# Optimization experiments

Measured on AMD Instinct MI355X. Metric: run time of the kernel, lower is better.

Reference implementation:

```python
import jax, jax.numpy as jnp
import numpy as np
from jax import lax

B, L = 2, 8192
HIDDEN = 2048
HEADS = 16
DPH = HIDDEN // HEADS          # hidden_size_per_attention_head = 128
STATE = 8                      # state_size
GROUPS = HIDDEN                # hyena_filter_groups == num_systems (per-channel filters)
K = 3                          # short_filter_length


def setup_inputs() -> dict:
    key = jax.random.key(0)
    ks = jax.random.split(key, 6)
    u = jax.random.normal(ks[0], (B, L, 3 * HIDDEN), jnp.float32)
    short_filter_weight = jax.random.normal(ks[1], (3 * HIDDEN, 1, K), jnp.float32) * 0.2
    short_filter_bias = jax.random.normal(ks[2], (3 * HIDDEN,), jnp.float32) * 0.1
    # poles must be stable (negative log-pole) so exp(log_pole * t) stays finite for t up to L
    log_poles = -jax.random.uniform(ks[3], (GROUPS, STATE, 1), jnp.float32, 1e-3, 0.1)
    residues = jax.random.normal(ks[4], (GROUPS, STATE), jnp.float32) * (1.0 / STATE)
    D = jax.random.normal(ks[5], (HIDDEN,), jnp.float32) * 0.1
    return {"u": u, "short_filter_weight": short_filter_weight,
            "short_filter_bias": short_filter_bias, "log_poles": log_poles,
            "residues": residues, "D": D}


def _column_split(z):
    # z: [B, 3*HIDDEN, L] -> head-wise split into x2, x1, v each [B, HIDDEN, L]
    b, _, l = z.shape
    z = z.reshape(b, HEADS, 3 * DPH, l)
    x2 = z[:, :, :DPH].reshape(b, HIDDEN, l)
    x1 = z[:, :, DPH:2 * DPH].reshape(b, HIDDEN, l)
    v = z[:, :, 2 * DPH:].reshape(b, HIDDEN, l)
    return x2, x1, v


def _forward(u, short_filter_weight, short_filter_bias, log_poles, residues, D):
    # ---- parallel_fir: causal depthwise short conv over 3*HIDDEN channels ----
    uc = jnp.transpose(u, (0, 2, 1))  # [B, 3D, L]
    z_pre = lax.conv_general_dilated(
        uc, short_filter_weight, window_strides=(1,), padding=[(K - 1, 0)],
        dimension_numbers=("NCH", "OIH", "NCH"), feature_group_count=3 * HIDDEN)
    z_pre = z_pre + short_filter_bias[None, :, None]  # [B, 3D, L]

    # ---- compute_filter: pole/residue SSM -> implicit long filter h [1, G, L] ----
    t = jnp.arange(L, dtype=jnp.float32)[None, None]            # [1, 1, L]
    kern = jnp.exp(log_poles * t)                               # [G, S, L]
    h = jnp.einsum("gs,gsl->gl", residues, kern)[None]          # [1, G, L]
    # repeat_interleave(hidden//groups = 1, dim=0) is a no-op when GROUPS == HIDDEN

    # ---- parallel_iir: column split, gating, FFT circular conv ----
    x2, x1, v = _column_split(z_pre)
    x1v = x1 * v                                                # [B, D, L]

    fft_size = 2 * L
    H = jnp.fft.rfft(h.astype(jnp.float32), n=fft_size) / fft_size
    X = jnp.fft.rfft(x1v.astype(jnp.float32), n=fft_size)
    y = jnp.fft.irfft(X * H, n=fft_size, norm="forward")[..., :L]
    y = (y.astype(x1v.dtype) + x1v * D[:, None]) * x2           # [B, D, L]
    return jnp.transpose(y, (0, 2, 1))                          # [B, L, D]


def reference(u, short_filter_weight, short_filter_bias, log_poles, residues, D):
    return _forward(u, short_filter_weight, short_filter_bias, log_poles, residues, D)
```

## Files before the change

### kernel.cpp

```cpp
#include <hip/hip_runtime.h>
#include <cstddef>

namespace {
constexpr int kB   = 2;
constexpr int kL   = 8192;
constexpr int kHid = 2048;
constexpr int kC3  = 6144;
constexpr int kS   = 8;
constexpr int kNC  = 64;
constexpr int kCL  = kL / kNC;
}

__global__ __launch_bounds__(256) void hyena_pass1(
    const float* __restrict__ u, const float* __restrict__ w,
    const float* __restrict__ bias, const float* __restrict__ lp,
    float* __restrict__ A)
{
  const int d  = blockIdx.x * 256 + threadIdx.x;
  const int ch = blockIdx.y;
  const int b  = blockIdx.z;
  const int head = d >> 7, r = d & 127;
  const int c1 = head * 384 + 128 + r;
  const int cv = head * 384 + 256 + r;

  const float w10 = w[c1*3+0], w11 = w[c1*3+1], w12 = w[c1*3+2], b1 = bias[c1];
  const float wv0 = w[cv*3+0], wv1 = w[cv*3+1], wv2 = w[cv*3+2], bv = bias[cv];

  float p[kS];
  #pragma unroll
  for (int j = 0; j < kS; ++j) p[j] = expf(lp[d*kS + j]);

  const int l0 = ch * kCL;
  const float* ub = u + (size_t)b * kL * kC3;

  float u1m2 = 0.f, u1m1 = 0.f, uvm2 = 0.f, uvm1 = 0.f;
  if (l0 >= 2) { u1m2 = ub[(size_t)(l0-2)*kC3 + c1]; uvm2 = ub[(size_t)(l0-2)*kC3 + cv]; }
  if (l0 >= 1) { u1m1 = ub[(size_t)(l0-1)*kC3 + c1]; uvm1 = ub[(size_t)(l0-1)*kC3 + cv]; }

  float s[kS];
  #pragma unroll
  for (int j = 0; j < kS; ++j) s[j] = 0.f;

  #pragma unroll 4
  for (int l = l0; l < l0 + kCL; ++l) {
    const float u1 = ub[(size_t)l*kC3 + c1];
    const float uv = ub[(size_t)l*kC3 + cv];
    const float x1 = fmaf(w10, u1m2, fmaf(w11, u1m1, fmaf(w12, u1, b1)));
    const float v  = fmaf(wv0, uvm2, fmaf(wv1, uvm1, fmaf(wv2, uv, bv)));
    const float x  = x1 * v;
    #pragma unroll
    for (int j = 0; j < kS; ++j) s[j] = fmaf(p[j], s[j], x);
    u1m2 = u1m1; u1m1 = u1; uvm2 = uvm1; uvm1 = uv;
  }

  float* Ad = A + (((size_t)b*kNC + ch)*kHid + d) * kS;
  #pragma unroll
  for (int j = 0; j < kS; ++j) Ad[j] = s[j];
}

__global__ __launch_bounds__(256) void hyena_pass2(
    const float* __restrict__ lp, float* __restrict__ A)
{
  const int t = blockIdx.x * 256 + threadIdx.x;
  const int j = t & (kS - 1);
  const int d = (t >> 3) & (kHid - 1);
  const int b = t >> 14;
  const float pC = expf(lp[d*kS + j] * (float)kCL);

  const size_t base   = (size_t)b * kNC * kHid * kS + (size_t)d * kS + j;
  const size_t stride = (size_t)kHid * kS;

  float s = 0.f;
  for (int c0 = 0; c0 < kNC; c0 += 8) {
    float a[8];
    #pragma unroll
    for (int k = 0; k < 8; ++k) a[k] = A[base + (size_t)(c0 + k) * stride];
    #pragma unroll
    for (int k = 0; k < 8; ++k) {
      s = fmaf(pC, s, a[k]);
      A[base + (size_t)(c0 + k) * stride] = s;
    }
  }
}

__global__ __launch_bounds__(256) void hyena_pass3(
    const float* __restrict__ u, const float* __restrict__ w,
    const float* __restrict__ bias, const float* __restrict__ lp,
    const float* __restrict__ res, const float* __restrict__ Dv,
    const float* __restrict__ A, float* __restrict__ out)
{
  const int d  = blockIdx.x * 256 + threadIdx.x;
  const int ch = blockIdx.y;
  const int b  = blockIdx.z;
  const int head = d >> 7, r = d & 127;
  const int c2 = head * 384 + r;
  const int c1 = c2 + 128;
  const int cv = c2 + 256;

  const float w20 = w[c2*3+0], w21 = w[c2*3+1], w22 = w[c2*3+2], b2 = bias[c2];
  const float w10 = w[c1*3+0], w11 = w[c1*3+1], w12 = w[c1*3+2], b1 = bias[c1];
  const float wv0 = w[cv*3+0], wv1 = w[cv*3+1], wv2 = w[cv*3+2], bv = bias[cv];
  const float Dd = Dv[d];

  float p[kS], rr[kS], s[kS];
  #pragma unroll
  for (int j = 0; j < kS; ++j) {
    p[j]  = expf(lp[d*kS + j]);
    rr[j] = res[d*kS + j];
  }
  if (ch == 0) {
    #pragma unroll
    for (int j = 0; j < kS; ++j) s[j] = 0.f;
  } else {
    const float* Ad = A + (((size_t)b*kNC + (ch - 1))*kHid + d) * kS;
    #pragma unroll
    for (int j = 0; j < kS; ++j) s[j] = Ad[j];
  }

  const int l0 = ch * kCL;
  const float* ub = u + (size_t)b * kL * kC3;

  float u2m2 = 0.f, u2m1 = 0.f, u1m2 = 0.f, u1m1 = 0.f, uvm2 = 0.f, uvm1 = 0.f;
  if (l0 >= 2) {
    u2m2 = ub[(size_t)(l0-2)*kC3 + c2];
    u1m2 = ub[(size_t)(l0-2)*kC3 + c1];
    uvm2 = ub[(size_t)(l0-2)*kC3 + cv];
  }
  if (l0 >= 1) {
    u2m1 = ub[(size_t)(l0-1)*kC3 + c2];
    u1m1 = ub[(size_t)(l0-1)*kC3 + c1];
    uvm1 = ub[(size_t)(l0-1)*kC3 + cv];
  }

  float* ob = out + (size_t)b * kL * kHid + d;

  #pragma unroll 4
  for (int l = l0; l < l0 + kCL; ++l) {
    const float u2 = ub[(size_t)l*kC3 + c2];
    const float u1 = ub[(size_t)l*kC3 + c1];
    const float uv = ub[(size_t)l*kC3 + cv];
    const float x2 = fmaf(w20, u2m2, fmaf(w21, u2m1, fmaf(w22, u2, b2)));
    const float x1 = fmaf(w10, u1m2, fmaf(w11, u1m1, fmaf(w12, u1, b1)));
    const float v  = fmaf(wv0, uvm2, fmaf(wv1, uvm1, fmaf(wv2, uv, bv)));
    const float x  = x1 * v;
    #pragma unroll
    for (int j = 0; j < kS; ++j) s[j] = fmaf(p[j], s[j], x);
    float y = 0.f;
    #pragma unroll
    for (int j = 0; j < kS; ++j) y = fmaf(rr[j], s[j], y);
    ob[(size_t)l * kHid] = fmaf(x, Dd, y) * x2;
    u2m2 = u2m1; u2m1 = u2; u1m2 = u1m1; u1m1 = u1; uvm2 = uvm1; uvm1 = uv;
  }
}

extern "C" void kernel_launch(void* const* d_in, const int* in_sizes, int n_in,
                              void* d_out, int out_size, void* d_ws, size_t ws_size,
                              hipStream_t stream) {
  const float* u    = (const float*)d_in[0];
  const float* w    = (const float*)d_in[1];
  const float* bias = (const float*)d_in[2];
  const float* lp   = (const float*)d_in[3];
  const float* res  = (const float*)d_in[4];
  const float* Dv   = (const float*)d_in[5];
  float* out = (float*)d_out;
  float* A   = (float*)d_ws;

  const dim3 blk(256);
  const dim3 g13(kHid / 256, kNC, kB);
  hipLaunchKernelGGL(hyena_pass1, g13, blk, 0, stream, u, w, bias, lp, A);
  hipLaunchKernelGGL(hyena_pass2, dim3((kB * kHid * kS) / 256), blk, 0, stream, lp, A);
  hipLaunchKernelGGL(hyena_pass3, g13, blk, 0, stream, u, w, bias, lp, res, Dv, A, out);
}
```

Baseline: 632.1 us.

## Process two channels per thread with float2 loads and double-buffered row prefetch

New measurement: 631.4 us. About the same (-0.1%).

```diff
diff --git a/kernel.cpp b/kernel.cpp
--- a/kernel.cpp
+++ b/kernel.cpp
@@ -1,5 +1,6 @@
 #include <hip/hip_runtime.h>
 #include <cstddef>
+#include <cstdint>
 
 namespace {
 constexpr int kB   = 2;
@@ -9,6 +10,8 @@
 constexpr int kS   = 8;
 constexpr int kNC  = 64;
 constexpr int kCL  = kL / kNC;
+constexpr int kRB  = 4;
+constexpr int kNB  = kCL / kRB;
 }
 
 __global__ __launch_bounds__(256) void hyena_pass1(
@@ -16,46 +19,100 @@
     const float* __restrict__ bias, const float* __restrict__ lp,
     float* __restrict__ A)
 {
-  const int d  = blockIdx.x * 256 + threadIdx.x;
-  const int ch = blockIdx.y;
-  const int b  = blockIdx.z;
-  const int head = d >> 7, r = d & 127;
-  const int c1 = head * 384 + 128 + r;
-  const int cv = head * 384 + 256 + r;
-
-  const float w10 = w[c1*3+0], w11 = w[c1*3+1], w12 = w[c1*3+2], b1 = bias[c1];
-  const float wv0 = w[cv*3+0], wv1 = w[cv*3+1], wv2 = w[cv*3+2], bv = bias[cv];
-
-  float p[kS];
-  #pragma unroll
-  for (int j = 0; j < kS; ++j) p[j] = expf(lp[d*kS + j]);
+  const int tid  = threadIdx.x;
+  const int ch   = blockIdx.y;
+  const int b    = blockIdx.z;
+  const int head = blockIdx.x * 4 + (tid >> 6);
+  const int r2   = (tid & 63) * 2;
+  const int d0   = head * 128 + r2;
+  const int c1   = head * 384 + 128 + r2;
+  const int cv   = c1 + 128;
+
+  float w1k[2][3], wvk[2][3], b1[2], bv[2];
+  #pragma unroll
+  for (int q = 0; q < 2; ++q) {
+    #pragma unroll
+    for (int k = 0; k < 3; ++k) {
+      w1k[q][k] = w[(c1 + q) * 3 + k];
+      wvk[q][k] = w[(cv + q) * 3 + k];
+    }
+    b1[q] = bias[c1 + q];
+    bv[q] = bias[cv + q];
+  }
+
+  float p[2][kS], s[2][kS];
+  #pragma unroll
+  for (int q = 0; q < 2; ++q)
+    #pragma unroll
+    for (int j = 0; j < kS; ++j) {
+      p[q][j] = expf(lp[(d0 + q) * kS + j]);
+      s[q][j] = 0.f;
+    }
 
   const int l0 = ch * kCL;
   const float* ub = u + (size_t)b * kL * kC3;
 
-  float u1m2 = 0.f, u1m1 = 0.f, uvm2 = 0.f, uvm1 = 0.f;
-  if (l0 >= 2) { u1m2 = ub[(size_t)(l0-2)*kC3 + c1]; uvm2 = ub[(size_t)(l0-2)*kC3 + cv]; }
-  if (l0 >= 1) { u1m1 = ub[(size_t)(l0-1)*kC3 + c1]; uvm1 = ub[(size_t)(l0-1)*kC3 + cv]; }
-
-  float s[kS];
-  #pragma unroll
-  for (int j = 0; j < kS; ++j) s[j] = 0.f;
-
-  #pragma unroll 4
-  for (int l = l0; l < l0 + kCL; ++l) {
-    const float u1 = ub[(size_t)l*kC3 + c1];
-    const float uv = ub[(size_t)l*kC3 + cv];
-    const float x1 = fmaf(w10, u1m2, fmaf(w11, u1m1, fmaf(w12, u1, b1)));
-    const float v  = fmaf(wv0, uvm2, fmaf(wv1, uvm1, fmaf(wv2, uv, bv)));
-    const float x  = x1 * v;
-    #pragma unroll
-    for (int j = 0; j < kS; ++j) s[j] = fmaf(p[j], s[j], x);
-    u1m2 = u1m1; u1m1 = u1; uvm2 = uvm1; uvm1 = uv;
-  }
-
-  float* Ad = A + (((size_t)b*kNC + ch)*kHid + d) * kS;
-  #pragma unroll
-  for (int j = 0; j < kS; ++j) Ad[j] = s[j];
+  float m2_1[2] = {0.f, 0.f}, m1_1[2] = {0.f, 0.f};
+  float m2_v[2] = {0.f, 0.f}, m1_v[2] = {0.f, 0.f};
+  if (l0 >= 2) {
+    float2 t1 = *(const float2*)&ub[(size_t)(l0 - 2) * kC3 + c1];
+    float2 tv = *(const float2*)&ub[(size_t)(l0 - 2) * kC3 + cv];
+    m2_1[0] = t1.x; m2_1[1] = t1.y; m2_v[0] = tv.x; m2_v[1] = tv.y;
+  }
+  if (l0 >= 1) {
+    float2 t1 = *(const float2*)&ub[(size_t)(l0 - 1) * kC3 + c1];
+    float2 tv = *(const float2*)&ub[(size_t)(l0 - 1) * kC3 + cv];
+    m1_1[0] = t1.x; m1_1[1] = t1.y; m1_v[0] = tv.x; m1_v[1] = tv.y;
+  }
+
+  const float* up = ub + (size_t)l0 * kC3;
+
+  float2 a1A[kRB], avA[kRB], a1B[kRB], avB[kRB];
+
+  auto loadb = [&](float2 (&a1)[kRB], float2 (&av)[kRB], int t) {
+    const float* rp = up + (size_t)t * kRB * kC3;
+    #pragma unroll
+    for (int k = 0; k < kRB; ++k) {
+      a1[k] = *(const float2*)&rp[(size_t)k * kC3 + c1];
+      av[k] = *(const float2*)&rp[(size_t)k * kC3 + cv];
+    }
+  };
+
+  auto comp = [&](const float2 (&a1)[kRB], const float2 (&av)[kRB]) {
+    #pragma unroll
+    for (int k = 0; k < kRB; ++k) {
+      const float c1v[2] = {a1[k].x, a1[k].y};
+      const float cvv[2] = {av[k].x, av[k].y};
+      #pragma unroll
+      for (int q = 0; q < 2; ++q) {
+        const float x1 = fmaf(w1k[q][0], m2_1[q],
+                         fmaf(w1k[q][1], m1_1[q],
+                         fmaf(w1k[q][2], c1v[q], b1[q])));
+        const float v  = fmaf(wvk[q][0], m2_v[q],
+                         fmaf(wvk[q][1], m1_v[q],
+                         fmaf(wvk[q][2], cvv[q], bv[q])));
+        const float x = x1 * v;
+        #pragma unroll
+        for (int j = 0; j < kS; ++j) s[q][j] = fmaf(p[q][j], s[q][j], x);
+        m2_1[q] = m1_1[q]; m1_1[q] = c1v[q];
+        m2_v[q] = m1_v[q]; m1_v[q] = cvv[q];
+      }
+    }
+  };
+
+  loadb(a1A, avA, 0);
+  for (int t = 0; t < kNB; t += 2) {
+    if (t + 1 < kNB) loadb(a1B, avB, t + 1);
+    comp(a1A, avA);
+    if (t + 2 < kNB) loadb(a1A, avA, t + 2);
+    comp(a1B, avB);
+  }
+
+  float* Ad = A + (((size_t)b * kNC + ch) * kHid + d0) * kS;
+  #pragma unroll
+  for (int q = 0; q < 2; ++q)
+    #pragma unroll
+    for (int j = 0; j < kS; ++j) Ad[q * kS + j] = s[q][j];
 }
 
 __global__ __launch_bounds__(256) void hyena_pass2(
@@ -89,67 +146,132 @@
     const float* __restrict__ res, const float* __restrict__ Dv,
     const float* __restrict__ A, float* __restrict__ out)
 {
-  const int d  = blockIdx.x * 256 + threadIdx.x;
-  const int ch = blockIdx.y;
-  const int b  = blockIdx.z;
-  const int head = d >> 7, r = d & 127;
-  const int c2 = head * 384 + r;
-  const int c1 = c2 + 128;
-  const int cv = c2 + 256;
-
-  const float w20 = w[c2*3+0], w21 = w[c2*3+1], w22 = w[c2*3+2], b2 = bias[c2];
-  const float w10 = w[c1*3+0], w11 = w[c1*3+1], w12 = w[c1*3+2], b1 = bias[c1];
-  const float wv0 = w[cv*3+0], wv1 = w[cv*3+1], wv2 = w[cv*3+2], bv = bias[cv];
-  const float Dd = Dv[d];
-
-  float p[kS], rr[kS], s[kS];
-  #pragma unroll
-  for (int j = 0; j < kS; ++j) {
-    p[j]  = expf(lp[d*kS + j]);
-    rr[j] = res[d*kS + j];
-  }
+  const int tid  = threadIdx.x;
+  const int ch   = blockIdx.y;
+  const int b    = blockIdx.z;
+  const int head = blockIdx.x * 4 + (tid >> 6);
+  const int r2   = (tid & 63) * 2;
+  const int d0   = head * 128 + r2;
+  const int c2   = head * 384 + r2;
+  const int c1   = c2 + 128;
+  const int cv   = c2 + 256;
+
+  float w2k[2][3], w1k[2][3], wvk[2][3], b2[2], b1[2], bv[2], Dd[2];
+  #pragma unroll
+  for (int q = 0; q < 2; ++q) {
+    #pragma unroll
+    for (int k = 0; k < 3; ++k) {
+      w2k[q][k] = w[(c2 + q) * 3 + k];
+      w1k[q][k] = w[(c1 + q) * 3 + k];
+      wvk[q][k] = w[(cv + q) * 3 + k];
+    }
+    b2[q] = bias[c2 + q];
+    b1[q] = bias[c1 + q];
+    bv[q] = bias[cv + q];
+    Dd[q] = Dv[d0 + q];
+  }
+
+  float p[2][kS], rr[2][kS], s[2][kS];
+  #pragma unroll
+  for (int q = 0; q < 2; ++q)
+    #pragma unroll
+    for (int j = 0; j < kS; ++j) {
+      p[q][j]  = expf(lp[(d0 + q) * kS + j]);
+      rr[q][j] = res[(d0 + q) * kS + j];
+    }
   if (ch == 0) {
     #pragma unroll
-    for (int j = 0; j < kS; ++j) s[j] = 0.f;
+    for (int q = 0; q < 2; ++q)
+      #pragma unroll
+      for (int j = 0; j < kS; ++j) s[q][j] = 0.f;
   } else {
-    const float* Ad = A + (((size_t)b*kNC + (ch - 1))*kHid + d) * kS;
-    #pragma unroll
-    for (int j = 0; j < kS; ++j) s[j] = Ad[j];
+    const float* Ad = A + (((size_t)b * kNC + (ch - 1)) * kHid + d0) * kS;
+    #pragma unroll
+    for (int q = 0; q < 2; ++q)
+      #pragma unroll
+      for (int j = 0; j < kS; ++j) s[q][j] = Ad[q * kS + j];
   }
 
   const int l0 = ch * kCL;
   const float* ub = u + (size_t)b * kL * kC3;
 
-  float u2m2 = 0.f, u2m1 = 0.f, u1m2 = 0.f, u1m1 = 0.f, uvm2 = 0.f, uvm1 = 0.f;
+  float m2_2[2] = {0.f, 0.f}, m1_2[2] = {0.f, 0.f};
+  float m2_1[2] = {0.f, 0.f}, m1_1[2] = {0.f, 0.f};
+  float m2_v[2] = {0.f, 0.f}, m1_v[2] = {0.f, 0.f};
   if (l0 >= 2) {
-    u2m2 = ub[(size_t)(l0-2)*kC3 + c2];
-    u1m2 = ub[(size_t)(l0-2)*kC3 + c1];
-    uvm2 = ub[(size_t)(l0-2)*kC3 + cv];
+    float2 t2 = *(const float2*)&ub[(size_t)(l0 - 2) * kC3 + c2];
+    float2 t1 = *(const float2*)&ub[(size_t)(l0 - 2) * kC3 + c1];
+    float2 tv = *(const float2*)&ub[(size_t)(l0 - 2) * kC3 + cv];
+    m2_2[0] = t2.x; m2_2[1] = t2.y;
+    m2_1[0] = t1.x; m2_1[1] = t1.y;
+    m2_v[0] = tv.x; m2_v[1] = tv.y;
   }
   if (l0 >= 1) {
-    u2m1 = ub[(size_t)(l0-1)*kC3 + c2];
-    u1m1 = ub[(size_t)(l0-1)*kC3 + c1];
-    uvm1 = ub[(size_t)(l0-1)*kC3 + cv];
-  }
-
-  float* ob = out + (size_t)b * kL * kHid + d;
-
-  #pragma unroll 4
-  for (int l = l0; l < l0 + kCL; ++l) {
-    const float u2 = ub[(size_t)l*kC3 + c2];
-    const float u1 = ub[(size_t)l*kC3 + c1];
-    const float uv = ub[(size_t)l*kC3 + cv];
-    const float x2 = fmaf(w20, u2m2, fmaf(w21, u2m1, fmaf(w22, u2, b2)));
-    const float x1 = fmaf(w10, u1m2, fmaf(w11, u1m1, fmaf(w12, u1, b1)));
-    const float v  = fmaf(wv0, uvm2, fmaf(wv1, uvm1, fmaf(wv2, uv, bv)));
-    const float x  = x1 * v;
-    #pragma unroll
-    for (int j = 0; j < kS; ++j) s[j] = fmaf(p[j], s[j], x);
-    float y = 0.f;
-    #pragma unroll
-    for (int j = 0; j < kS; ++j) y = fmaf(rr[j], s[j], y);
-    ob[(size_t)l * kHid] = fmaf(x, Dd, y) * x2;
-    u2m2 = u2m1; u2m1 = u2; u1m2 = u1m1; u1m1 = u1; uvm2 = uvm1; uvm1 = uv;
+    float2 t2 = *(const float2*)&ub[(size_t)(l0 - 1) * kC3 + c2];
+    float2 t1 = *(const float2*)&ub[(size_t)(l0 - 1) * kC3 + c1];
+    float2 tv = *(const float2*)&ub[(size_t)(l0 - 1) * kC3 + cv];
+    m1_2[0] = t2.x; m1_2[1] = t2.y;
+    m1_1[0] = t1.x; m1_1[1] = t1.y;
+    m1_v[0] = tv.x; m1_v[1] = tv.y;
+  }
+
+  const float* up = ub + (size_t)l0 * kC3;
+  float* ob = out + ((size_t)b * kL + l0) * kHid + d0;
+
+  float2 a2A[kRB], a1A[kRB], avA[kRB];
+  float2 a2B[kRB], a1B[kRB], avB[kRB];
+
+  auto loadb = [&](float2 (&a2)[kRB], float2 (&a1)[kRB], float2 (&av)[kRB],
+                   int t) {
+    const float* rp = up + (size_t)t * kRB * kC3;
+    #pragma unroll
+    for (int k = 0; k < kRB; ++k) {
+      a2[k] = *(const float2*)&rp[(size_t)k * kC3 + c2];
+      a1[k] = *(const float2*)&rp[(size_t)k * kC3 + c1];
+      av[k] = *(const float2*)&rp[(size_t)k * kC3 + cv];
+    }
+  };
+
+  auto comp = [&](const float2 (&a2)[kRB], const float2 (&a1)[kRB],
+                  const float2 (&av)[kRB], int t) {
+    #pragma unroll
+    for (int k = 0; k < kRB; ++k) {
+      const float c2v[2] = {a2[k].x, a2[k].y};
+      const float c1v[2] = {a1[k].x, a1[k].y};
+      const float cvv[2] = {av[k].x, av[k].y};
+      float o[2];
+      #pragma unroll
+      for (int q = 0; q < 2; ++q) {
+        const float x2 = fmaf(w2k[q][0], m2_2[q],
+                         fmaf(w2k[q][1], m1_2[q],
+                         fmaf(w2k[q][2], c2v[q], b2[q])));
+        const float x1 = fmaf(w1k[q][0], m2_1[q],
+                         fmaf(w1k[q][1], m1_1[q],
+                         fmaf(w1k[q][2], c1v[q], b1[q])));
+        const float v  = fmaf(wvk[q][0], m2_v[q],
+                         fmaf(wvk[q][1], m1_v[q],
+                         fmaf(wvk[q][2], cvv[q], bv[q])));
+        const float x = x1 * v;
+        #pragma unroll
+        for (int j = 0; j < kS; ++j) s[q][j] = fmaf(p[q][j], s[q][j], x);
+        float y = 0.f;
+        #pragma unroll
+        for (int j = 0; j < kS; ++j) y = fmaf(rr[q][j], s[q][j], y);
+        o[q] = fmaf(x, Dd[q], y) * x2;
+        m2_2[q] = m1_2[q]; m1_2[q] = c2v[q];
+        m2_1[q] = m1_1[q]; m1_1[q] = c1v[q];
+        m2_v[q] = m1_v[q]; m1_v[q] = cvv[q];
+      }
+      *(float2*)&ob[(size_t)(t * kRB + k) * kHid] = make_float2(o[0], o[1]);
+    }
+  };
+
+  loadb(a2A, a1A, avA, 0);
+  for (int t = 0; t < kNB; t += 2) {
+    if (t + 1 < kNB) loadb(a2B, a1B, avB, t + 1);
+    comp(a2A, a1A, avA, t);
+    if (t + 2 < kNB) loadb(a2A, a1A, avA, t + 2);
+    comp(a2B, a1B, avB, t + 1);
   }
 }
 
@@ -166,7 +288,7 @@
   float* A   = (float*)d_ws;
 
   const dim3 blk(256);
-  const dim3 g13(kHid / 256, kNC, kB);
+  const dim3 g13(kHid / 512, kNC, kB);
   hipLaunchKernelGGL(hyena_pass1, g13, blk, 0, stream, u, w, bias, lp, A);
   hipLaunchKernelGGL(hyena_pass2, dim3((kB * kHid * kS) / 256), blk, 0, stream, lp, A);
   hipLaunchKernelGGL(hyena_pass3, g13, blk, 0, stream, u, w, bias, lp, res, Dv, A, out);
```

## Fuse three scan passes into one kernel with grid barrier and fp16-cached gated input

Applied to the files above, without the earlier changes.

New measurement: 785.7 us. 24.3% more time.

```diff
diff --git a/kernel.cpp b/kernel.cpp
--- a/kernel.cpp
+++ b/kernel.cpp
@@ -1,155 +1,145 @@
 #include <hip/hip_runtime.h>
+#include <hip/hip_fp16.h>
 #include <cstddef>
+#include <cstdint>
 
 namespace {
-constexpr int kB   = 2;
-constexpr int kL   = 8192;
-constexpr int kHid = 2048;
-constexpr int kC3  = 6144;
-constexpr int kS   = 8;
-constexpr int kNC  = 64;
-constexpr int kCL  = kL / kNC;
+constexpr int kB    = 2;
+constexpr int kL    = 8192;
+constexpr int kHid  = 2048;
+constexpr int kC3   = 6144;
+constexpr int kS    = 8;
+constexpr int kNC   = 32;
+constexpr int kCL   = kL / kNC;
+constexpr int kPair = kCL / 2;
+constexpr unsigned kNBlk = kB * kNC * 8;
 }
 
-__global__ __launch_bounds__(256) void hyena_pass1(
+__global__ __launch_bounds__(256, 2) void hyena_fused(
     const float* __restrict__ u, const float* __restrict__ w,
     const float* __restrict__ bias, const float* __restrict__ lp,
-    float* __restrict__ A)
+    const float* __restrict__ res, const float* __restrict__ Dv,
+    float* __restrict__ A, unsigned* __restrict__ cnt,
+    float* __restrict__ out)
 {
-  const int d  = blockIdx.x * 256 + threadIdx.x;
-  const int ch = blockIdx.y;
-  const int b  = blockIdx.z;
-  const int head = d >> 7, r = d & 127;
-  const int c1 = head * 384 + 128 + r;
-  const int cv = head * 384 + 256 + r;
+  const int tid   = threadIdx.x;
+  const int slice = blockIdx.x & 7;
+  const int ch    = (blockIdx.x >> 3) & 31;
+  const int b     = blockIdx.x >> 8;
+  const int d     = slice * 256 + tid;
+  const int head  = d >> 7;
+  const int c2    = head * 384 + (d & 127);
+  const int c1    = c2 + 128;
+  const int cv    = c2 + 256;
 
   const float w10 = w[c1*3+0], w11 = w[c1*3+1], w12 = w[c1*3+2], b1 = bias[c1];
   const float wv0 = w[cv*3+0], wv1 = w[cv*3+1], wv2 = w[cv*3+2], bv = bias[cv];
 
-  float p[kS];
+  float p[kS], s[kS];
   #pragma unroll
-  for (int j = 0; j < kS; ++j) p[j] = expf(lp[d*kS + j]);
+  for (int j = 0; j < kS; ++j) { p[j] = expf(lp[d*kS + j]); s[j] = 0.f; }
 
   const int l0 = ch * kCL;
   const float* ub = u + (size_t)b * kL * kC3;
+  const float* up = ub + (size_t)l0 * kC3;
 
-  float u1m2 = 0.f, u1m1 = 0.f, uvm2 = 0.f, uvm1 = 0.f;
-  if (l0 >= 2) { u1m2 = ub[(size_t)(l0-2)*kC3 + c1]; uvm2 = ub[(size_t)(l0-2)*kC3 + cv]; }
-  if (l0 >= 1) { u1m1 = ub[(size_t)(l0-1)*kC3 + c1]; uvm1 = ub[(size_t)(l0-1)*kC3 + cv]; }
+  float m2 = 0.f, m1 = 0.f, n2 = 0.f, n1 = 0.f;
+  if (l0 >= 2) { m2 = ub[(size_t)(l0-2)*kC3 + c1]; n2 = ub[(size_t)(l0-2)*kC3 + cv]; }
+  if (l0 >= 1) { m1 = ub[(size_t)(l0-1)*kC3 + c1]; n1 = ub[(size_t)(l0-1)*kC3 + cv]; }
 
-  float s[kS];
+  __half2 xv[kPair];
   #pragma unroll
-  for (int j = 0; j < kS; ++j) s[j] = 0.f;
-
-  #pragma unroll 4
-  for (int l = l0; l < l0 + kCL; ++l) {
-    const float u1 = ub[(size_t)l*kC3 + c1];
-    const float uv = ub[(size_t)l*kC3 + cv];
-    const float x1 = fmaf(w10, u1m2, fmaf(w11, u1m1, fmaf(w12, u1, b1)));
-    const float v  = fmaf(wv0, uvm2, fmaf(wv1, uvm1, fmaf(wv2, uv, bv)));
-    const float x  = x1 * v;
+  for (int k = 0; k < kPair; ++k) {
+    const float a0 = up[(size_t)(2*k  )*kC3 + c1];
+    const float e0 = up[(size_t)(2*k  )*kC3 + cv];
+    const float a1 = up[(size_t)(2*k+1)*kC3 + c1];
+    const float e1 = up[(size_t)(2*k+1)*kC3 + cv];
+    const float x1a = fmaf(w10, m2, fmaf(w11, m1, fmaf(w12, a0, b1)));
+    const float vva = fmaf(wv0, n2, fmaf(wv1, n1, fmaf(wv2, e0, bv)));
+    const float x0  = x1a * vva;
     #pragma unroll
-    for (int j = 0; j < kS; ++j) s[j] = fmaf(p[j], s[j], x);
-    u1m2 = u1m1; u1m1 = u1; uvm2 = uvm1; uvm1 = uv;
+    for (int j = 0; j < kS; ++j) s[j] = fmaf(p[j], s[j], x0);
+    const float x1b = fmaf(w10, m1, fmaf(w11, a0, fmaf(w12, a1, b1)));
+    const float vvb = fmaf(wv0, n1, fmaf(wv1, e0, fmaf(wv2, e1, bv)));
+    const float x1v1 = x1b * vvb;
+    #pragma unroll
+    for (int j = 0; j < kS; ++j) s[j] = fmaf(p[j], s[j], x1v1);
+    m2 = a0; m1 = a1; n2 = e0; n1 = e1;
+    xv[k] = __float22half2_rn(make_float2(x0, x1v1));
   }
 
-  float* Ad = A + (((size_t)b*kNC + ch)*kHid + d) * kS;
-  #pragma unroll
-  for (int j = 0; j < kS; ++j) Ad[j] = s[j];
-}
+  {
+    float* Ad = A + (((size_t)b * kNC + ch) * kHid + d) * kS;
+    #pragma unroll
+    for (int j = 0; j < kS; ++j) Ad[j] = s[j];
+  }
 
-__global__ __launch_bounds__(256) void hyena_pass2(
-    const float* __restrict__ lp, float* __restrict__ A)
-{
-  const int t = blockIdx.x * 256 + threadIdx.x;
-  const int j = t & (kS - 1);
-  const int d = (t >> 3) & (kHid - 1);
-  const int b = t >> 14;
-  const float pC = expf(lp[d*kS + j] * (float)kCL);
-
-  const size_t base   = (size_t)b * kNC * kHid * kS + (size_t)d * kS + j;
-  const size_t stride = (size_t)kHid * kS;
-
-  float s = 0.f;
-  for (int c0 = 0; c0 < kNC; c0 += 8) {
-    float a[8];
-    #pragma unroll
-    for (int k = 0; k < 8; ++k) a[k] = A[base + (size_t)(c0 + k) * stride];
-    #pragma unroll
-    for (int k = 0; k < 8; ++k) {
-      s = fmaf(pC, s, a[k]);
-      A[base + (size_t)(c0 + k) * stride] = s;
+  __syncthreads();
+  if (tid == 0) {
+    __hip_atomic_fetch_add(cnt, 1u, __ATOMIC_ACQ_REL, __HIP_MEMORY_SCOPE_AGENT);
+    unsigned long guard = 0;
+    while (__hip_atomic_load(cnt, __ATOMIC_ACQUIRE,
+                             __HIP_MEMORY_SCOPE_AGENT) < kNBlk) {
+      __builtin_amdgcn_s_sleep(2);
+      if (++guard > (1ul << 27)) break;
     }
   }
-}
+  __syncthreads();
 
-__global__ __launch_bounds__(256) void hyena_pass3(
-    const float* __restrict__ u, const float* __restrict__ w,
-    const float* __restrict__ bias, const float* __restrict__ lp,
-    const float* __restrict__ res, const float* __restrict__ Dv,
-    const float* __restrict__ A, float* __restrict__ out)
-{
-  const int d  = blockIdx.x * 256 + threadIdx.x;
-  const int ch = blockIdx.y;
-  const int b  = blockIdx.z;
-  const int head = d >> 7, r = d & 127;
-  const int c2 = head * 384 + r;
-  const int c1 = c2 + 128;
-  const int cv = c2 + 256;
+  float si[kS];
+  #pragma unroll
+  for (int j = 0; j < kS; ++j) si[j] = 0.f;
+  {
+    float pC[kS];
+    #pragma unroll
+    for (int j = 0; j < kS; ++j) pC[j] = expf(lp[d*kS + j] * (float)kCL);
+    for (int c = 0; c < ch; ++c) {
+      const float* Ac = A + (((size_t)b * kNC + c) * kHid + d) * kS;
+      const float4 q0 = *(const float4*)Ac;
+      const float4 q1 = *(const float4*)(Ac + 4);
+      si[0] = fmaf(pC[0], si[0], q0.x);
+      si[1] = fmaf(pC[1], si[1], q0.y);
+      si[2] = fmaf(pC[2], si[2], q0.z);
+      si[3] = fmaf(pC[3], si[3], q0.w);
+      si[4] = fmaf(pC[4], si[4], q1.x);
+      si[5] = fmaf(pC[5], si[5], q1.y);
+      si[6] = fmaf(pC[6], si[6], q1.z);
+      si[7] = fmaf(pC[7], si[7], q1.w);
+    }
+  }
 
   const float w20 = w[c2*3+0], w21 = w[c2*3+1], w22 = w[c2*3+2], b2 = bias[c2];
-  const float w10 = w[c1*3+0], w11 = w[c1*3+1], w12 = w[c1*3+2], b1 = bias[c1];
-  const float wv0 = w[cv*3+0], wv1 = w[cv*3+1], wv2 = w[cv*3+2], bv = bias[cv];
   const float Dd = Dv[d];
+  float rr[kS];
+  #pragma unroll
+  for (int j = 0; j < kS; ++j) rr[j] = res[d*kS + j];
 
-  float p[kS], rr[kS], s[kS];
+  float g2 = 0.f, g1 = 0.f;
+  if (l0 >= 2) g2 = ub[(size_t)(l0-2)*kC3 + c2];
+  if (l0 >= 1) g1 = ub[(size_t)(l0-1)*kC3 + c2];
+
+  float* ob = out + ((size_t)b * kL + l0) * kHid + d;
+
   #pragma unroll
-  for (int j = 0; j < kS; ++j) {
-    p[j]  = expf(lp[d*kS + j]);
-    rr[j] = res[d*kS + j];
-  }
-  if (ch == 0) {
+  for (int k = 0; k < kPair; ++k) {
+    const float z0 = up[(size_t)(2*k  )*kC3 + c2];
+    const float z1 = up[(size_t)(2*k+1)*kC3 + c2];
+    const float2 xf = __half22float2(xv[k]);
+    const float x2a = fmaf(w20, g2, fmaf(w21, g1, fmaf(w22, z0, b2)));
+    const float x2b = fmaf(w20, g1, fmaf(w21, z0, fmaf(w22, z1, b2)));
     #pragma unroll
-    for (int j = 0; j < kS; ++j) s[j] = 0.f;
-  } else {
-    const float* Ad = A + (((size_t)b*kNC + (ch - 1))*kHid + d) * kS;
+    for (int j = 0; j < kS; ++j) si[j] = fmaf(p[j], si[j], xf.x);
+    float y0 = 0.f;
     #pragma unroll
-    for (int j = 0; j < kS; ++j) s[j] = Ad[j];
-  }
-
-  const int l0 = ch * kCL;
-  const float* ub = u + (size_t)b * kL * kC3;
-
-  float u2m2 = 0.f, u2m1 = 0.f, u1m2 = 0.f, u1m1 = 0.f, uvm2 = 0.f, uvm1 = 0.f;
-  if (l0 >= 2) {
-    u2m2 = ub[(size_t)(l0-2)*kC3 + c2];
-    u1m2 = ub[(size_t)(l0-2)*kC3 + c1];
-    uvm2 = ub[(size_t)(l0-2)*kC3 + cv];
-  }
-  if (l0 >= 1) {
-    u2m1 = ub[(size_t)(l0-1)*kC3 + c2];
-    u1m1 = ub[(size_t)(l0-1)*kC3 + c1];
-    uvm1 = ub[(size_t)(l0-1)*kC3 + cv];
-  }
-
-  float* ob = out + (size_t)b * kL * kHid + d;
-
-  #pragma unroll 4
-  for (int l = l0; l < l0 + kCL; ++l) {
-    const float u2 = ub[(size_t)l*kC3 + c2];
-    const float u1 = ub[(size_t)l*kC3 + c1];
-    const float uv = ub[(size_t)l*kC3 + cv];
-    const float x2 = fmaf(w20, u2m2, fmaf(w21, u2m1, fmaf(w22, u2, b2)));
-    const float x1 = fmaf(w10, u1m2, fmaf(w11, u1m1, fmaf(w12, u1, b1)));
-    const float v  = fmaf(wv0, uvm2, fmaf(wv1, uvm1, fmaf(wv2, uv, bv)));
-    const float x  = x1 * v;
+    for (int j = 0; j < kS; ++j) y0 = fmaf(rr[j], si[j], y0);
+    ob[(size_t)(2*k) * kHid] = fmaf(xf.x, Dd, y0) * x2a;
     #pragma unroll
-    for (int j = 0; j < kS; ++j) s[j] = fmaf(p[j], s[j], x);
-    float y = 0.f;
+    for (int j = 0; j < kS; ++j) si[j] = fmaf(p[j], si[j], xf.y);
+    float y1 = 0.f;
     #pragma unroll
-    for (int j = 0; j < kS; ++j) y = fmaf(rr[j], s[j], y);
-    ob[(size_t)l * kHid] = fmaf(x, Dd, y) * x2;
-    u2m2 = u2m1; u2m1 = u2; u1m2 = u1m1; u1m1 = u1; uvm2 = uvm1; uvm1 = uv;
+    for (int j = 0; j < kS; ++j) y1 = fmaf(rr[j], si[j], y1);
+    ob[(size_t)(2*k+1) * kHid] = fmaf(xf.y, Dd, y1) * x2b;
+    g2 = z0; g1 = z1;
   }
 }
 
@@ -164,10 +154,9 @@
   const float* Dv   = (const float*)d_in[5];
   float* out = (float*)d_out;
   float* A   = (float*)d_ws;
+  unsigned* cnt = (unsigned*)((char*)d_ws + (size_t)kB * kNC * kHid * kS * 4);
 
-  const dim3 blk(256);
-  const dim3 g13(kHid / 256, kNC, kB);
-  hipLaunchKernelGGL(hyena_pass1, g13, blk, 0, stream, u, w, bias, lp, A);
-  hipLaunchKernelGGL(hyena_pass2, dim3((kB * kHid * kS) / 256), blk, 0, stream, lp, A);
-  hipLaunchKernelGGL(hyena_pass3, g13, blk, 0, stream, u, w, bias, lp, res, Dv, A, out);
+  hipMemsetAsync(cnt, 0, sizeof(unsigned), stream);
+  hipLaunchKernelGGL(hyena_fused, dim3(kNBlk), dim3(256), 0, stream,
+                     u, w, bias, lp, res, Dv, A, cnt, out);
 }
```
